# Optimization experiments

Measured on AMD Instinct MI355X. Metric: run time of the kernel, lower is better.

The kernel has to match this reference:

```python
import jax, jax.numpy as jnp
import numpy as np

# Faithful reference for NaiveKmeans._cost / one assignment step of forward:
# squared Euclidean distances (torch.cdist(x, centers)**2) followed by a
# row-wise min (costs) and argmin (cluster indices).
# Note: the original module's host-side while-loop re-seeds centers as
# x[indices] (shape (N,d)), which is a bug that explodes to an NxN cdist;
# the kernel-relevant, well-defined math is this single cdist^2 + min step,
# which we implement here (it is exactly what forward computes before the loop).

def setup_inputs() -> dict:
    key = jax.random.key(0)
    kx, kc = jax.random.split(key)
    x = jax.random.normal(kx, (131072, 128), dtype=jnp.float32)
    centers = jax.random.normal(kc, (1024, 128), dtype=jnp.float32)
    return {"x": x, "centers": centers}


def _sq_cdist(x, c):
    x2 = jnp.sum(x * x, axis=1, keepdims=True)        # [N, 1]
    c2 = jnp.sum(c * c, axis=1)                       # [K]
    d2 = x2 + c2 - 2.0 * (x @ c.T)                    # [N, K]
    return jnp.maximum(d2, 0.0)


def reference(x, centers):
    d2 = _sq_cdist(x, centers)          # [N, K] squared distances
    costs = jnp.min(d2, axis=1)         # [N] per-point cost
    indices = jnp.argmin(d2, axis=1)    # [N] cluster assignment
    return costs, indices
```

## Files before the change

kernel.cpp:

```cpp
#include <hip/hip_runtime.h>


typedef _Float16 f16x8 __attribute__((ext_vector_type(8)));
typedef float    f32x4 __attribute__((ext_vector_type(4)));
typedef unsigned short u16;

constexpr int N = 131072, D = 128, K = 1024;
constexpr int MT = 128;

union H2U { _Float16 h; unsigned short u; };

__device__ inline void gl_lds16(const void* g, void* l) {
  __builtin_amdgcn_global_load_lds(
      (const __attribute__((address_space(1))) unsigned int*)g,
      (__attribute__((address_space(3))) unsigned int*)l, 16, 0, 0);
}

__global__ void prep_centers(const float* __restrict__ centers,
                             u16* __restrict__ Bh, u16* __restrict__ Bl,
                             float* __restrict__ c2) {
  const int wave = threadIdx.x >> 6, lane = threadIdx.x & 63;
  const int c = blockIdx.x * 4 + wave;
  const float2 v = ((const float2*)(centers + (size_t)c * D))[lane];
  float s = v.x * v.x + v.y * v.y;
  #pragma unroll
  for (int off = 32; off; off >>= 1) s += __shfl_xor(s, off, 64);
  if (lane == 0) c2[c] = s;

  H2U h0, h1, l0, l1;
  h0.h = (_Float16)v.x;  l0.h = (_Float16)(v.x - (float)h0.h);
  h1.h = (_Float16)v.y;  l1.h = (_Float16)(v.y - (float)h1.h);
  const int cb = c >> 7, cm = c & 127;
  const int kc = lane >> 4, q = (lane >> 2) & 3, j0 = (lane & 3) * 2;
  const size_t off = (((size_t)(cb * 4 + kc) * 4 + q) * 128 + cm) * 8 + j0;
  *(unsigned*)(Bh + off) = (unsigned)h0.u | ((unsigned)h1.u << 16);
  *(unsigned*)(Bl + off) = (unsigned)l0.u | ((unsigned)l1.u << 16);
}

__global__ __launch_bounds__(256, 2) void kmeans_mfma(
    const float* __restrict__ x,
    const u16* __restrict__ Bh_g, const u16* __restrict__ Bl_g,
    const float* __restrict__ c2g,
    float* __restrict__ out_cost, float* __restrict__ out_idx)
{
  __shared__ __align__(16) u16 Ah[16384];
  __shared__ __align__(16) u16 Al[16384];
  __shared__ __align__(16) u16 Bbuf[8192];

  const int tid = threadIdx.x;
  const int wave = tid >> 6, lane = tid & 63;
  const int wr = wave >> 1, wc = wave & 1;
  const int q = lane >> 4, ln = lane & 15;
  const int m0 = blockIdx.x * MT;

  #pragma unroll
  for (int i = 0; i < 16; ++i) {
    const int flat = i * 256 + tid;
    const int m = flat >> 5, c4 = flat & 31, k0 = c4 * 4;
    const float4 v = *(const float4*)(x + (size_t)(m0 + m) * D + k0);
    const int kc = k0 >> 5, qq = (k0 >> 3) & 3, j0 = k0 & 7;
    const float vv[4] = {v.x, v.y, v.z, v.w};
    H2U h[4], l[4];
    #pragma unroll
    for (int z = 0; z < 4; ++z) {
      h[z].h = (_Float16)vv[z];
      l[z].h = (_Float16)(vv[z] - (float)h[z].h);
    }
    const int off = ((kc * 4 + qq) * 128 + m) * 8 + j0;
    uint2 hp, lp;
    hp.x = h[0].u | ((unsigned)h[1].u << 16); hp.y = h[2].u | ((unsigned)h[3].u << 16);
    lp.x = l[0].u | ((unsigned)l[1].u << 16); lp.y = l[2].u | ((unsigned)l[3].u << 16);
    *(uint2*)(Ah + off) = hp;
    *(uint2*)(Al + off) = lp;
  }
  __syncthreads();

  float x2m = 0.f;
  if (tid < MT) {
    #pragma unroll
    for (int kq = 0; kq < 16; ++kq) {
      const f16x8 hv = *(const f16x8*)(Ah + (kq * 128 + tid) * 8);
      const f16x8 lv = *(const f16x8*)(Al + (kq * 128 + tid) * 8);
      #pragma unroll
      for (int e = 0; e < 8; ++e) {
        const float xv = (float)hv[e] + (float)lv[e];
        x2m += xv * xv;
      }
    }
  }

  float bestV[16]; int bestI[16];
  #pragma unroll
  for (int b = 0; b < 16; ++b) { bestV[b] = 3.4e38f; bestI[b] = 0; }

  for (int ct = 0; ct < 8; ++ct) {
    f32x4 acc[4][4];
    #pragma unroll
    for (int mt = 0; mt < 4; ++mt)
      #pragma unroll
      for (int nt = 0; nt < 4; ++nt)
        acc[mt][nt] = (f32x4){0.f, 0.f, 0.f, 0.f};

    for (int kc = 0; kc < 4; ++kc) {
      __syncthreads();
      {
        const size_t gbase = (size_t)(ct * 4 + kc) * 4096;
        #pragma unroll
        for (int i = 0; i < 2; ++i) {
          const size_t eoff = (size_t)i * 2048 + (size_t)wave * 512;
          gl_lds16(Bh_g + gbase + eoff + (size_t)lane * 8, Bbuf + eoff);
          gl_lds16(Bl_g + gbase + eoff + (size_t)lane * 8, Bbuf + 4096 + eoff);
        }
      }
      __syncthreads();

      f16x8 ah[4], al[4], bh[4], bl[4];
      #pragma unroll
      for (int t = 0; t < 4; ++t) {
        const int moff = ((kc * 4 + q) * 128 + wr * 64 + t * 16 + ln) * 8;
        ah[t] = *(const f16x8*)(Ah + moff);
        al[t] = *(const f16x8*)(Al + moff);
        const int noff = (q * 128 + wc * 64 + t * 16 + ln) * 8;
        bh[t] = *(const f16x8*)(Bbuf + noff);
        bl[t] = *(const f16x8*)(Bbuf + 4096 + noff);
      }
      #pragma unroll
      for (int mt = 0; mt < 4; ++mt)
        #pragma unroll
        for (int nt = 0; nt < 4; ++nt)
          acc[mt][nt] = __builtin_amdgcn_mfma_f32_16x16x32_f16(ah[mt], bh[nt], acc[mt][nt], 0, 0, 0);
      #pragma unroll
      for (int mt = 0; mt < 4; ++mt)
        #pragma unroll
        for (int nt = 0; nt < 4; ++nt)
          acc[mt][nt] = __builtin_amdgcn_mfma_f32_16x16x32_f16(al[mt], bh[nt], acc[mt][nt], 0, 0, 0);
      #pragma unroll
      for (int mt = 0; mt < 4; ++mt)
        #pragma unroll
        for (int nt = 0; nt < 4; ++nt)
          acc[mt][nt] = __builtin_amdgcn_mfma_f32_16x16x32_f16(ah[mt], bl[nt], acc[mt][nt], 0, 0, 0);
    }

    #pragma unroll
    for (int nt = 0; nt < 4; ++nt) {
      const int n = ct * 128 + wc * 64 + nt * 16 + ln;
      const float c2v = c2g[n];
      #pragma unroll
      for (int mt = 0; mt < 4; ++mt)
        #pragma unroll
        for (int r = 0; r < 4; ++r) {
          const float s = __builtin_fmaf(-2.f, acc[mt][nt][r], c2v);
          const int b = mt * 4 + r;
          if (s < bestV[b]) { bestV[b] = s; bestI[b] = n; }
        }
    }
  }

  #pragma unroll
  for (int b = 0; b < 16; ++b) {
    float v = bestV[b]; int idx = bestI[b];
    #pragma unroll
    for (int off = 1; off < 16; off <<= 1) {
      const float ov = __shfl_xor(v, off, 64);
      const int   oi = __shfl_xor(idx, off, 64);
      if (ov < v || (ov == v && oi < idx)) { v = ov; idx = oi; }
    }
    bestV[b] = v; bestI[b] = idx;
  }

  __syncthreads();
  float* redV = (float*)Bbuf;
  int*   redI = (int*)(Bbuf + 4096);
  if (ln == 0) {
    #pragma unroll
    for (int b = 0; b < 16; ++b) {
      const int ml = wr * 64 + (b >> 2) * 16 + q * 4 + (b & 3);
      redV[ml * 2 + wc] = bestV[b];
      redI[ml * 2 + wc] = bestI[b];
    }
  }
  __syncthreads();
  if (tid < MT) {
    float v = redV[tid * 2]; int idx = redI[tid * 2];
    const float v1 = redV[tid * 2 + 1]; const int i1 = redI[tid * 2 + 1];
    if (v1 < v || (v1 == v && i1 < idx)) { v = v1; idx = i1; }
    float cost = x2m + v;
    if (cost < 0.f) cost = 0.f;
    out_cost[m0 + tid] = cost;
    out_idx[m0 + tid]  = (float)idx;
  }
}

extern "C" void kernel_launch(void* const* d_in, const int* in_sizes, int n_in,
                              void* d_out, int out_size, void* d_ws, size_t ws_size,
                              hipStream_t stream) {
  const float* x       = (const float*)d_in[0];
  const float* centers = (const float*)d_in[1];
  u16*   Bh = (u16*)d_ws;
  u16*   Bl = Bh + (size_t)K * D;
  float* c2 = (float*)(Bl + (size_t)K * D);
  float* out_cost = (float*)d_out;
  float* out_idx  = out_cost + N;

  prep_centers<<<K / 4, 256, 0, stream>>>(centers, Bh, Bl, c2);
  kmeans_mfma<<<N / MT, 256, 0, stream>>>(x, Bh, Bl, c2, out_cost, out_idx);
}
```

Baseline: 183.1 us.

## Load center fragments directly from global into registers, drop LDS staging and barriers

Removes the LDS staging buffer for the center fragments. Each wave now reads its f16x8 B fragments straight from global memory (L2/L1-resident), which removes two __syncthreads per k-chunk and lets the k loop unroll. The center norms are also cached in LDS once per block. The trade-off is duplicated global traffic, since both waves sharing a column tile load the same fragments, and more exposed global-load latency with no explicit prefetch.

```diff
diff --git a/kernel.cpp b/kernel.cpp
--- a/kernel.cpp
+++ b/kernel.cpp
@@ -9,12 +9,6 @@
 constexpr int MT = 128;
 
 union H2U { _Float16 h; unsigned short u; };
-
-__device__ inline void gl_lds16(const void* g, void* l) {
-  __builtin_amdgcn_global_load_lds(
-      (const __attribute__((address_space(1))) unsigned int*)g,
-      (__attribute__((address_space(3))) unsigned int*)l, 16, 0, 0);
-}
 
 __global__ void prep_centers(const float* __restrict__ centers,
                              u16* __restrict__ Bh, u16* __restrict__ Bl,
@@ -45,7 +39,9 @@
 {
   __shared__ __align__(16) u16 Ah[16384];
   __shared__ __align__(16) u16 Al[16384];
-  __shared__ __align__(16) u16 Bbuf[8192];
+  __shared__ float c2l[K];
+  __shared__ float redV[256];
+  __shared__ int   redI[256];
 
   const int tid = threadIdx.x;
   const int wave = tid >> 6, lane = tid & 63;
@@ -73,6 +69,7 @@
     *(uint2*)(Ah + off) = hp;
     *(uint2*)(Al + off) = lp;
   }
+  for (int i = tid; i < K; i += 256) c2l[i] = c2g[i];
   __syncthreads();
 
   float x2m = 0.f;
@@ -101,28 +98,18 @@
       for (int nt = 0; nt < 4; ++nt)
         acc[mt][nt] = (f32x4){0.f, 0.f, 0.f, 0.f};
 
+    #pragma unroll
     for (int kc = 0; kc < 4; ++kc) {
-      __syncthreads();
-      {
-        const size_t gbase = (size_t)(ct * 4 + kc) * 4096;
-        #pragma unroll
-        for (int i = 0; i < 2; ++i) {
-          const size_t eoff = (size_t)i * 2048 + (size_t)wave * 512;
-          gl_lds16(Bh_g + gbase + eoff + (size_t)lane * 8, Bbuf + eoff);
-          gl_lds16(Bl_g + gbase + eoff + (size_t)lane * 8, Bbuf + 4096 + eoff);
-        }
-      }
-      __syncthreads();
-
       f16x8 ah[4], al[4], bh[4], bl[4];
       #pragma unroll
       for (int t = 0; t < 4; ++t) {
+        const size_t noff =
+            ((size_t)((ct * 4 + kc) * 4 + q) * 128 + wc * 64 + t * 16 + ln) * 8;
+        bh[t] = *(const f16x8*)(Bh_g + noff);
+        bl[t] = *(const f16x8*)(Bl_g + noff);
         const int moff = ((kc * 4 + q) * 128 + wr * 64 + t * 16 + ln) * 8;
         ah[t] = *(const f16x8*)(Ah + moff);
         al[t] = *(const f16x8*)(Al + moff);
-        const int noff = (q * 128 + wc * 64 + t * 16 + ln) * 8;
-        bh[t] = *(const f16x8*)(Bbuf + noff);
-        bl[t] = *(const f16x8*)(Bbuf + 4096 + noff);
       }
       #pragma unroll
       for (int mt = 0; mt < 4; ++mt)
@@ -144,7 +131,7 @@
     #pragma unroll
     for (int nt = 0; nt < 4; ++nt) {
       const int n = ct * 128 + wc * 64 + nt * 16 + ln;
-      const float c2v = c2g[n];
+      const float c2v = c2l[n];
       #pragma unroll
       for (int mt = 0; mt < 4; ++mt)
         #pragma unroll
@@ -168,9 +155,6 @@
     bestV[b] = v; bestI[b] = idx;
   }
 
-  __syncthreads();
-  float* redV = (float*)Bbuf;
-  int*   redI = (int*)(Bbuf + 4096);
   if (ln == 0) {
     #pragma unroll
     for (int b = 0; b < 16; ++b) {
```

After: 307.1 us. +67.7%, slower.

## Double-buffer center tiles in LDS and prefetch low halves into registers

Applied to the files above, without the earlier changes.

Each k-chunk of the high-half center tile is now staged into one of two LDS buffers. The next chunk is issued right after the single per-iteration barrier, so its load overlaps the current MFMA work. The low-half center fragments are read straight from global memory into registers one chunk ahead, and the c2 values are hoisted ahead of the k loop. This removes one barrier per chunk and cuts LDS traffic. In exchange it adds register pressure, and correctness relies on the barrier waiting for the outstanding LDS-direct loads.

```diff
diff --git a/kernel.cpp b/kernel.cpp
--- a/kernel.cpp
+++ b/kernel.cpp
@@ -43,9 +43,9 @@
     const float* __restrict__ c2g,
     float* __restrict__ out_cost, float* __restrict__ out_idx)
 {
-  __shared__ __align__(16) u16 Ah[16384];
-  __shared__ __align__(16) u16 Al[16384];
-  __shared__ __align__(16) u16 Bbuf[8192];
+  __shared__ __align__(16) u16 smem[40960];
+  u16* Ah = smem;
+  u16* Al = smem + 16384;
 
   const int tid = threadIdx.x;
   const int wave = tid >> 6, lane = tid & 63;
@@ -89,9 +89,28 @@
     }
   }
 
+  auto stageBh = [&](int cc, int p) {
+    const size_t gbase = (size_t)cc * 4096;
+    u16* buf = smem + 32768 + p * 4096;
+    #pragma unroll
+    for (int i = 0; i < 2; ++i) {
+      const size_t eoff = (size_t)i * 2048 + (size_t)wave * 512;
+      gl_lds16(Bh_g + gbase + eoff + (size_t)lane * 8, buf + eoff);
+    }
+  };
+  auto blPtr = [&](int cc, int t) {
+    return (const f16x8*)(Bl_g +
+        ((size_t)(cc * 4 + q) * 128 + wc * 64 + t * 16 + ln) * 8);
+  };
+
   float bestV[16]; int bestI[16];
   #pragma unroll
   for (int b = 0; b < 16; ++b) { bestV[b] = 3.4e38f; bestI[b] = 0; }
+
+  stageBh(0, 0);
+  f16x8 blc[4], bln[4];
+  #pragma unroll
+  for (int t = 0; t < 4; ++t) blc[t] = *blPtr(0, t);
 
   for (int ct = 0; ct < 8; ++ct) {
     f32x4 acc[4][4];
@@ -101,28 +120,29 @@
       for (int nt = 0; nt < 4; ++nt)
         acc[mt][nt] = (f32x4){0.f, 0.f, 0.f, 0.f};
 
+    float c2v[4];
+    #pragma unroll
+    for (int nt = 0; nt < 4; ++nt)
+      c2v[nt] = c2g[ct * 128 + wc * 64 + nt * 16 + ln];
+
+    #pragma unroll
     for (int kc = 0; kc < 4; ++kc) {
+      const int cc = ct * 4 + kc;
       __syncthreads();
-      {
-        const size_t gbase = (size_t)(ct * 4 + kc) * 4096;
-        #pragma unroll
-        for (int i = 0; i < 2; ++i) {
-          const size_t eoff = (size_t)i * 2048 + (size_t)wave * 512;
-          gl_lds16(Bh_g + gbase + eoff + (size_t)lane * 8, Bbuf + eoff);
-          gl_lds16(Bl_g + gbase + eoff + (size_t)lane * 8, Bbuf + 4096 + eoff);
-        }
+      if (cc < 31) {
+        stageBh(cc + 1, (cc + 1) & 1);
+        #pragma unroll
+        for (int t = 0; t < 4; ++t) bln[t] = *blPtr(cc + 1, t);
       }
-      __syncthreads();
-
-      f16x8 ah[4], al[4], bh[4], bl[4];
+      const u16* buf = smem + 32768 + (cc & 1) * 4096;
+
+      f16x8 ah[4], al[4], bh[4];
       #pragma unroll
       for (int t = 0; t < 4; ++t) {
         const int moff = ((kc * 4 + q) * 128 + wr * 64 + t * 16 + ln) * 8;
         ah[t] = *(const f16x8*)(Ah + moff);
         al[t] = *(const f16x8*)(Al + moff);
-        const int noff = (q * 128 + wc * 64 + t * 16 + ln) * 8;
-        bh[t] = *(const f16x8*)(Bbuf + noff);
-        bl[t] = *(const f16x8*)(Bbuf + 4096 + noff);
+        bh[t] = *(const f16x8*)(buf + (q * 128 + wc * 64 + t * 16 + ln) * 8);
       }
       #pragma unroll
       for (int mt = 0; mt < 4; ++mt)
@@ -138,18 +158,19 @@
       for (int mt = 0; mt < 4; ++mt)
         #pragma unroll
         for (int nt = 0; nt < 4; ++nt)
-          acc[mt][nt] = __builtin_amdgcn_mfma_f32_16x16x32_f16(ah[mt], bl[nt], acc[mt][nt], 0, 0, 0);
+          acc[mt][nt] = __builtin_amdgcn_mfma_f32_16x16x32_f16(ah[mt], blc[nt], acc[mt][nt], 0, 0, 0);
+      #pragma unroll
+      for (int t = 0; t < 4; ++t) blc[t] = bln[t];
     }
 
     #pragma unroll
     for (int nt = 0; nt < 4; ++nt) {
       const int n = ct * 128 + wc * 64 + nt * 16 + ln;
-      const float c2v = c2g[n];
       #pragma unroll
       for (int mt = 0; mt < 4; ++mt)
         #pragma unroll
         for (int r = 0; r < 4; ++r) {
-          const float s = __builtin_fmaf(-2.f, acc[mt][nt][r], c2v);
+          const float s = __builtin_fmaf(-2.f, acc[mt][nt][r], c2v[nt]);
           const int b = mt * 4 + r;
           if (s < bestV[b]) { bestV[b] = s; bestI[b] = n; }
         }
@@ -169,8 +190,8 @@
   }
 
   __syncthreads();
-  float* redV = (float*)Bbuf;
-  int*   redI = (int*)(Bbuf + 4096);
+  float* redV = (float*)(smem + 32768);
+  int*   redI = (int*)(smem + 33280);
   if (ln == 0) {
     #pragma unroll
     for (int b = 0; b < 16; ++b) {
```

After: 179.4 us. -2.0%, faster.
